# Performance work log

Measured on AMD Instinct MI355X. Metric: run time of the kernel, lower is better.

Reference implementation:

```python
import jax, jax.numpy as jnp
import numpy as np

E = 1024
H = 16
HD = E // H
FF = 4 * E
B, T = 2, 2048


def _linear_params(key, fan_in, fan_out):
    k1, k2 = jax.random.split(key)
    bound = 1.0 / np.sqrt(fan_in)
    W = jax.random.uniform(k1, (fan_out, fan_in), jnp.float32, -bound, bound)
    b = jax.random.uniform(k2, (fan_out,), jnp.float32, -bound, bound)
    return W, b


def setup_inputs() -> dict:
    key = jax.random.key(0)
    keys = jax.random.split(key, 8)
    x = jax.random.normal(keys[0], (B, T, E), jnp.float32)
    Wq, bq = _linear_params(keys[1], E, E)
    Wk, bk = _linear_params(keys[2], E, E)
    Wv, bv = _linear_params(keys[3], E, E)
    Wo, bo = _linear_params(keys[4], E, E)
    W1, b1 = _linear_params(keys[5], E, FF)
    W2, b2 = _linear_params(keys[6], FF, E)
    ln1_g = jnp.ones((E,), jnp.float32); ln1_b = jnp.zeros((E,), jnp.float32)
    ln2_g = jnp.ones((E,), jnp.float32); ln2_b = jnp.zeros((E,), jnp.float32)
    return {"x": x, "Wq": Wq, "bq": bq, "Wk": Wk, "bk": bk, "Wv": Wv, "bv": bv,
            "Wo": Wo, "bo": bo, "W1": W1, "b1": b1, "W2": W2, "b2": b2,
            "ln1_g": ln1_g, "ln1_b": ln1_b, "ln2_g": ln2_g, "ln2_b": ln2_b}


def _layernorm(x, g, b, eps=1e-5):
    mu = jnp.mean(x, axis=-1, keepdims=True)
    var = jnp.var(x, axis=-1, keepdims=True)
    return (x - mu) * jax.lax.rsqrt(var + eps) * g + b


def reference(x, Wq, bq, Wk, bk, Wv, bv, Wo, bo, W1, b1, W2, b2,
              ln1_g, ln1_b, ln2_g, ln2_b):
    Bc, Tc, Ec = x.shape
    h = _layernorm(x, ln1_g, ln1_b)
    # projections (torch Linear: y = x @ W.T + b)
    q = (h @ Wq.T + bq).reshape(Bc, Tc, H, HD).transpose(0, 2, 1, 3)  # [B,H,T,hd]
    k = (h @ Wk.T + bk).reshape(Bc, Tc, H, HD).transpose(0, 2, 1, 3)
    v = (h @ Wv.T + bv).reshape(Bc, Tc, H, HD).transpose(0, 2, 1, 3)
    scores = jnp.einsum('bhqd,bhkd->bhqk', q, k) / np.sqrt(HD).astype(np.float32)
    causal = jnp.tril(jnp.ones((Tc, Tc), bool))
    scores = jnp.where(causal, scores, -jnp.inf)
    att = jax.nn.softmax(scores, axis=-1)  # dropout = identity (eval)
    out = jnp.einsum('bhqk,bhkd->bhqd', att, v)
    out = out.transpose(0, 2, 1, 3).reshape(Bc, Tc, Ec)
    x = x + out @ Wo.T + bo
    h2 = _layernorm(x, ln2_g, ln2_b)
    ff = jax.nn.relu(h2 @ W1.T + b1) @ W2.T + b2
    return x + ff
```

## Files before the change

### kernel.cpp

```cpp
#include <hip/hip_runtime.h>

typedef unsigned short u16;
typedef __bf16 bf16x8 __attribute__((ext_vector_type(8)));
typedef float f32x4 __attribute__((ext_vector_type(4)));

#define E_ 1024
#define T_ 2048
#define B_ 2
#define H_ 16
#define FF_ 4096
#define M_ 4096

__device__ __forceinline__ u16 f2b(float f) {
    union { float f; unsigned u; } c; c.f = f;
    unsigned r = c.u + 0x7FFFu + ((c.u >> 16) & 1u);
    return (u16)(r >> 16);
}
__device__ __forceinline__ u16 f2bt(float f) {
    union { float f; unsigned u; } c; c.f = f;
    return (u16)(c.u >> 16);
}

__device__ __forceinline__ void gl16(const u16* g, u16* l) {
    __builtin_amdgcn_global_load_lds(
        (__attribute__((address_space(1))) void*)g,
        (__attribute__((address_space(3))) void*)l, 16, 0, 0);
}

template<int N> __device__ __forceinline__ void wait_vmcnt() {
    if constexpr (N == 2)      asm volatile("s_waitcnt vmcnt(2)" ::: "memory");
    else if constexpr (N == 3) asm volatile("s_waitcnt vmcnt(3)" ::: "memory");
    else if constexpr (N == 4) asm volatile("s_waitcnt vmcnt(4)" ::: "memory");
    else                       asm volatile("s_waitcnt vmcnt(0)" ::: "memory");
}

__global__ __launch_bounds__(256) void cvt_ln(
        const float* __restrict__ Wq, const float* __restrict__ Wk,
        const float* __restrict__ Wv, const float* __restrict__ Wo,
        const float* __restrict__ W1, const float* __restrict__ W2,
        const float* __restrict__ bq, const float* __restrict__ bk,
        const float* __restrict__ bv,
        u16* __restrict__ WqkvB, u16* __restrict__ WoB,
        u16* __restrict__ W1B, u16* __restrict__ W2B,
        float* __restrict__ bqkv,
        const float* __restrict__ x, const float* __restrict__ g1,
        const float* __restrict__ b1v, u16* __restrict__ hB) {
    if (blockIdx.x < 1024) {
        int row = blockIdx.x * 4 + (threadIdx.x >> 6);
        int t = threadIdx.x & 63;
        const float* xr = x + (size_t)row * E_;
        float v[16];
        float sum = 0.f, ss = 0.f;
#pragma unroll
        for (int c = 0; c < 4; c++) {
            float4 f = *(const float4*)&xr[c * 256 + t * 4];
            v[c * 4 + 0] = f.x; v[c * 4 + 1] = f.y; v[c * 4 + 2] = f.z; v[c * 4 + 3] = f.w;
            sum += f.x + f.y + f.z + f.w;
            ss += f.x * f.x + f.y * f.y + f.z * f.z + f.w * f.w;
        }
#pragma unroll
        for (int d = 32; d; d >>= 1) {
            sum += __shfl_xor(sum, d);
            ss  += __shfl_xor(ss, d);
        }
        float mu = sum * (1.f / E_);
        float var = ss * (1.f / E_) - mu * mu;
        float rs = rsqrtf(var + 1e-5f);
#pragma unroll
        for (int c = 0; c < 4; c++) {
            int idx = c * 256 + t * 4;
            float4 g4 = *(const float4*)&g1[idx];
            float4 b4 = *(const float4*)&b1v[idx];
            ushort4 o;
            o.x = f2b((v[c * 4 + 0] - mu) * rs * g4.x + b4.x);
            o.y = f2b((v[c * 4 + 1] - mu) * rs * g4.y + b4.y);
            o.z = f2b((v[c * 4 + 2] - mu) * rs * g4.z + b4.z);
            o.w = f2b((v[c * 4 + 3] - mu) * rs * g4.w + b4.w);
            *(ushort4*)&hB[(size_t)row * E_ + idx] = o;
        }
        return;
    }
    int i = (blockIdx.x - 1024) * 256 + threadIdx.x;
    if (i >= 3146496) return;
    if (i >= 3145728) {
        int j = i - 3145728;
        const float* s = (j < 256) ? bq : (j < 512) ? bk : bv;
        int jj = j & 255;
        *(float4*)&bqkv[j * 4] = *(const float4*)&s[jj * 4];
        return;
    }
    const float* src; u16* dst; int j;
    if (i < 786432) {
        src = (i < 262144) ? Wq : (i < 524288) ? Wk : Wv;
        j = i & 262143;
        dst = WqkvB + (i >> 18) * (E_ * E_);
    } else if (i < 1048576) { j = i - 786432;  src = Wo; dst = WoB; }
    else if (i < 2097152)   { j = i - 1048576; src = W1; dst = W1B; }
    else                    { j = i - 2097152; src = W2; dst = W2B; }
    float4 f = *(const float4*)&src[j * 4];
    ushort4 o;
    o.x = f2b(f.x); o.y = f2b(f.y); o.z = f2b(f.z); o.w = f2b(f.w);
    *(ushort4*)&dst[j * 4] = o;
}

__global__ __launch_bounds__(64) void ln_fwd(u16* __restrict__ out, const float* __restrict__ x,
                                             const float* __restrict__ g, const float* __restrict__ bta) {
    int row = blockIdx.x;
    int t = threadIdx.x;
    const float* xr = x + (size_t)row * E_;
    float v[16];
    float sum = 0.f, ss = 0.f;
#pragma unroll
    for (int c = 0; c < 4; c++) {
        float4 f = *(const float4*)&xr[c * 256 + t * 4];
        v[c * 4 + 0] = f.x; v[c * 4 + 1] = f.y; v[c * 4 + 2] = f.z; v[c * 4 + 3] = f.w;
        sum += f.x + f.y + f.z + f.w;
        ss += f.x * f.x + f.y * f.y + f.z * f.z + f.w * f.w;
    }
#pragma unroll
    for (int d = 32; d; d >>= 1) {
        sum += __shfl_xor(sum, d);
        ss  += __shfl_xor(ss, d);
    }
    float mu = sum * (1.f / E_);
    float var = ss * (1.f / E_) - mu * mu;
    float rs = rsqrtf(var + 1e-5f);
#pragma unroll
    for (int c = 0; c < 4; c++) {
        int idx = c * 256 + t * 4;
        float4 g4 = *(const float4*)&g[idx];
        float4 b4 = *(const float4*)&bta[idx];
        ushort4 o;
        o.x = f2b((v[c * 4 + 0] - mu) * rs * g4.x + b4.x);
        o.y = f2b((v[c * 4 + 1] - mu) * rs * g4.y + b4.y);
        o.z = f2b((v[c * 4 + 2] - mu) * rs * g4.z + b4.z);
        o.w = f2b((v[c * 4 + 3] - mu) * rs * g4.w + b4.w);
        *(ushort4*)&out[(size_t)row * E_ + idx] = o;
    }
}

template<int BM, int BN>
__global__ __launch_bounds__(256) void gemm_bt(
        const u16* __restrict__ A, const u16* __restrict__ Bt,
        const float* __restrict__ bias, const float* __restrict__ residual,
        float* __restrict__ outF, float* __restrict__ outF1,
        u16* __restrict__ outB, u16* __restrict__ outVt,
        int M, int N, int K, int ldk, int relu, int qkvmode) {
    constexpr int MT = BM / 32, NT = BN / 32;
    constexpr int LA = BM / 64, LB = BN / 64;
    __shared__ __align__(16) u16 As[3][BM * 32];
    __shared__ __align__(16) u16 Bs[3][BN * 32];
    int tid = threadIdx.x;
    int m0 = blockIdx.y * BM, n0 = blockIdx.x * BN;
    int kz = blockIdx.z;
    int koff = kz * K;
    int wave = tid >> 6, lane = tid & 63;
    int wm = wave & 1, wn = wave >> 1;
    int r16 = lane & 15, kg = lane >> 4;

    const u16* gA = A + (size_t)(m0 + wave * (BM / 4) + (lane >> 2)) * ldk + koff + (lane & 3) * 8;
    const u16* gB = Bt + (size_t)(n0 + wave * (BN / 4) + (lane >> 2)) * ldk + koff + (lane & 3) * 8;
    size_t row16 = (size_t)16 * ldk;
    int aoff = wave * (BM / 4) * 32;
    int boff = wave * (BN / 4) * 32;

    f32x4 acc[MT][NT] = {};

    const int nk = K >> 5;

    auto issue = [&](int kt, int buf) {
        int k1 = kt << 5;
        gl16(gA + k1, As[buf] + aoff);
        if (LA == 2) gl16(gA + k1 + row16, As[buf] + aoff + 512);
        gl16(gB + k1, Bs[buf] + boff);
        if (LB == 2) gl16(gB + k1 + row16, Bs[buf] + boff + 512);
    };

    auto compute = [&](int cb) {
        bf16x8 af[MT], bfr[NT];
#pragma unroll
        for (int mt = 0; mt < MT; mt++)
            af[mt] = *(const bf16x8*)&As[cb][(wm * (BM / 2) + mt * 16 + r16) * 32 + kg * 8];
#pragma unroll
        for (int nt = 0; nt < NT; nt++)
            bfr[nt] = *(const bf16x8*)&Bs[cb][(wn * (BN / 2) + nt * 16 + r16) * 32 + kg * 8];
#pragma unroll
        for (int mt = 0; mt < MT; mt++)
#pragma unroll
            for (int nt = 0; nt < NT; nt++)
                acc[mt][nt] = __builtin_amdgcn_mfma_f32_16x16x32_bf16(af[mt], bfr[nt], acc[mt][nt], 0, 0, 0);
    };

    issue(0, 0);
    issue(1, 1);

    int cur = 0;
    for (int ks = 0; ks < nk - 1; ks++) {
        wait_vmcnt<LA + LB>();
        __builtin_amdgcn_s_barrier();
        asm volatile("" ::: "memory");
        if (ks + 2 < nk) {
            int p2 = cur ? cur - 1 : 2;
            issue(ks + 2, p2);
        }
        compute(cur);
        cur = (cur < 2) ? cur + 1 : 0;
    }
    asm volatile("s_waitcnt vmcnt(0)" ::: "memory");
    __builtin_amdgcn_s_barrier();
    asm volatile("" ::: "memory");
    compute(cur);

#pragma unroll
    for (int mt = 0; mt < MT; mt++) {
#pragma unroll
        for (int nt = 0; nt < NT; nt++) {
            int gm = m0 + wm * (BM / 2) + mt * 16 + kg * 4;
            int gn = n0 + wn * (BN / 2) + nt * 16 + r16;
            float bv = bias[gn];
            if (qkvmode) {
                if (gn < 2048) {
                    float scl = (gn < 1024) ? 0.18033688f : 1.0f;
#pragma unroll
                    for (int r = 0; r < 4; r++)
                        outB[(size_t)(gm + r) * 2048 + gn] = f2b((acc[mt][nt][r] + bv) * scl);
                } else {
                    int bq_ = gm >> 11, tq = gm & 2047, d = gn - 2048;
                    ushort4 ov;
                    ov.x = f2b(acc[mt][nt][0] + bv);
                    ov.y = f2b(acc[mt][nt][1] + bv);
                    ov.z = f2b(acc[mt][nt][2] + bv);
                    ov.w = f2b(acc[mt][nt][3] + bv);
                    *(ushort4*)&outVt[((size_t)(bq_ * 1024 + d)) * 2048 + tq] = ov;
                }
            } else if (outF1) {
#pragma unroll
                for (int r = 0; r < 4; r++) {
                    size_t off = (size_t)(gm + r) * N + gn;
                    if (kz == 0) {
                        float v = acc[mt][nt][r] + bv;
                        if (residual) v += residual[off];
                        outF[off] = v;
                    } else {
                        outF1[off] = acc[mt][nt][r];
                    }
                }
            } else {
#pragma unroll
                for (int r = 0; r < 4; r++) {
                    float v = acc[mt][nt][r] + bv;
                    size_t off = (size_t)(gm + r) * N + gn;
                    if (residual) v += residual[off];
                    if (relu) v = fmaxf(v, 0.f);
                    if (outF) outF[off] = v;
                    else outB[off] = f2b(v);
                }
            }
        }
    }
}

__global__ __launch_bounds__(256) void addf4(float* __restrict__ d, const float* __restrict__ p) {
    size_t i = ((size_t)blockIdx.x * 256 + threadIdx.x) * 4;
    float4 a = *(float4*)&d[i];
    float4 b = *(const float4*)&p[i];
    a.x += b.x; a.y += b.y; a.z += b.z; a.w += b.w;
    *(float4*)&d[i] = a;
}

#define AST 68
__global__ __launch_bounds__(256) void attn_mfma(
        const u16* __restrict__ qk, const u16* __restrict__ vt,
        u16* __restrict__ out) {
    __shared__ __align__(16) u16 Ks[2][64 * AST];
    __shared__ __align__(16) u16 Vs[2][64 * AST];
    __shared__ __align__(16) u16 Ps[4][16 * AST];

    int bz = blockIdx.x;
    int h  = bz & 15;
    int b  = (bz >> 4) & 1;
    int qt = bz >> 5;

    int tid = threadIdx.x;
    int w = tid >> 6, lane = tid & 63;
    int g = lane >> 4, l16 = lane & 15;

    int qrow = qt * 64 + w * 16 + l16;
    bf16x8 qf[2];
    qf[0] = *(const bf16x8*)&qk[(size_t)(b * T_ + qrow) * 2048 + h * 64 + g * 8];
    qf[1] = *(const bf16x8*)&qk[(size_t)(b * T_ + qrow) * 2048 + h * 64 + 32 + g * 8];

    f32x4 o[4] = {};
    f32x4 lp = {0.f, 0.f, 0.f, 0.f};

    int r1 = tid >> 3, col1 = (tid & 7) * 8;
    const u16* gK = qk + (size_t)(b * T_) * 2048 + 1024 + h * 64;
    const u16* gV = vt + (size_t)(b * 1024 + h * 64) * 2048;

    uint4 kr1 = *(const uint4*)&gK[(size_t)r1 * 2048 + col1];
    uint4 kr2 = *(const uint4*)&gK[(size_t)(r1 + 32) * 2048 + col1];
    uint4 vr1 = *(const uint4*)&gV[(size_t)r1 * 2048 + col1];
    uint4 vr2 = *(const uint4*)&gV[(size_t)(r1 + 32) * 2048 + col1];

    for (int t = 0; t <= qt; t++) {
        int cur = t & 1;
        *(uint4*)&Ks[cur][r1 * AST + col1] = kr1;
        *(uint4*)&Ks[cur][(r1 + 32) * AST + col1] = kr2;
        *(uint4*)&Vs[cur][r1 * AST + col1] = vr1;
        *(uint4*)&Vs[cur][(r1 + 32) * AST + col1] = vr2;
        __syncthreads();
        if (t < qt) {
            int j1 = (t + 1) * 64;
            kr1 = *(const uint4*)&gK[(size_t)(j1 + r1) * 2048 + col1];
            kr2 = *(const uint4*)&gK[(size_t)(j1 + r1 + 32) * 2048 + col1];
            vr1 = *(const uint4*)&gV[(size_t)r1 * 2048 + j1 + col1];
            vr2 = *(const uint4*)&gV[(size_t)(r1 + 32) * 2048 + j1 + col1];
        }

        f32x4 s[4];
#pragma unroll
        for (int nt = 0; nt < 4; nt++) {
            f32x4 c16 = {-16.f, -16.f, -16.f, -16.f};
            bf16x8 k0 = *(const bf16x8*)&Ks[cur][(nt * 16 + l16) * AST + g * 8];
            bf16x8 k1 = *(const bf16x8*)&Ks[cur][(nt * 16 + l16) * AST + 32 + g * 8];
            s[nt] = __builtin_amdgcn_mfma_f32_16x16x32_bf16(qf[0], k0, c16, 0, 0, 0);
            s[nt] = __builtin_amdgcn_mfma_f32_16x16x32_bf16(qf[1], k1, s[nt], 0, 0, 0);
        }

        if (t == qt) {
            int j0 = t * 64;
#pragma unroll
            for (int nt = 0; nt < 4; nt++) {
                int key = j0 + nt * 16 + l16;
#pragma unroll
                for (int r = 0; r < 4; r++) {
                    int q = qt * 64 + w * 16 + g * 4 + r;
                    if (key > q) s[nt][r] = -INFINITY;
                }
            }
        }

#pragma unroll
        for (int nt = 0; nt < 4; nt++)
#pragma unroll
            for (int r = 0; r < 4; r++) {
                float p = exp2f(s[nt][r]);
                lp[r] += p;
                Ps[w][(g * 4 + r) * AST + nt * 16 + l16] = f2bt(p);
            }

#pragma unroll
        for (int kf = 0; kf < 2; kf++) {
            bf16x8 pf = *(const bf16x8*)&Ps[w][l16 * AST + kf * 32 + g * 8];
#pragma unroll
            for (int nt = 0; nt < 4; nt++) {
                bf16x8 vf = *(const bf16x8*)&Vs[cur][(nt * 16 + l16) * AST + kf * 32 + g * 8];
                o[nt] = __builtin_amdgcn_mfma_f32_16x16x32_bf16(pf, vf, o[nt], 0, 0, 0);
            }
        }
    }

#pragma unroll
    for (int x = 1; x <= 8; x <<= 1)
#pragma unroll
        for (int r = 0; r < 4; r++)
            lp[r] += __shfl_xor(lp[r], x);

    float inv[4];
#pragma unroll
    for (int r = 0; r < 4; r++) inv[r] = 1.f / lp[r];
    int qg = qt * 64 + w * 16 + g * 4;
#pragma unroll
    for (int nt = 0; nt < 4; nt++)
#pragma unroll
        for (int r = 0; r < 4; r++)
            out[(size_t)(b * T_ + qg + r) * E_ + h * 64 + nt * 16 + l16] =
                f2b(o[nt][r] * inv[r]);
}

extern "C" void kernel_launch(void* const* d_in, const int* in_sizes, int n_in,
                              void* d_out, int out_size, void* d_ws, size_t ws_size,
                              hipStream_t stream) {
    const float* x    = (const float*)d_in[0];
    const float* Wq   = (const float*)d_in[1];
    const float* bq   = (const float*)d_in[2];
    const float* Wk   = (const float*)d_in[3];
    const float* bk   = (const float*)d_in[4];
    const float* Wv   = (const float*)d_in[5];
    const float* bv   = (const float*)d_in[6];
    const float* Wo   = (const float*)d_in[7];
    const float* bo   = (const float*)d_in[8];
    const float* W1   = (const float*)d_in[9];
    const float* b1   = (const float*)d_in[10];
    const float* W2   = (const float*)d_in[11];
    const float* b2   = (const float*)d_in[12];
    const float* ln1g = (const float*)d_in[13];
    const float* ln1b = (const float*)d_in[14];
    const float* ln2g = (const float*)d_in[15];
    const float* ln2b = (const float*)d_in[16];

    char* ws = (char*)d_ws;
    size_t off = 0;
    auto alloc = [&](size_t bytes) { char* p = ws + off; off += (bytes + 255) & ~(size_t)255; return p; };

    u16*   hB    = (u16*)  alloc((size_t)M_ * E_ * 2);
    u16*   WqkvB = (u16*)  alloc((size_t)3 * E_ * E_ * 2);
    u16*   WoB   = (u16*)  alloc((size_t)E_ * E_ * 2);
    u16*   W1B   = (u16*)  alloc((size_t)FF_ * E_ * 2);
    u16*   W2B   = (u16*)  alloc((size_t)E_ * FF_ * 2);
    float* bqkv  = (float*)alloc(3 * E_ * 4);
    u16*   qkB   = (u16*)  alloc((size_t)M_ * 2 * E_ * 2);
    u16*   vtG   = (u16*)  alloc((size_t)M_ * E_ * 2);
    u16*   attnB = (u16*)  alloc((size_t)M_ * E_ * 2);
    float* x2    = (float*)alloc((size_t)M_ * E_ * 4);
    u16*   h2B   = (u16*)  alloc((size_t)M_ * E_ * 2);
    u16*   rB    = (u16*)  alloc((size_t)M_ * FF_ * 2);
    float* P1    = (float*)alloc((size_t)M_ * E_ * 4);

    cvt_ln<<<1024 + 12291, 256, 0, stream>>>(Wq, Wk, Wv, Wo, W1, W2, bq, bk, bv,
                                             WqkvB, WoB, W1B, W2B, bqkv,
                                             x, ln1g, ln1b, hB);

    gemm_bt<128, 128><<<dim3(3 * E_ / 128, M_ / 128), 256, 0, stream>>>(
        hB, WqkvB, bqkv, nullptr, nullptr, nullptr, qkB, vtG, M_, 3 * E_, E_, E_, 0, 1);

    attn_mfma<<<B_ * H_ * (T_ / 64), 256, 0, stream>>>(qkB, vtG, attnB);

    gemm_bt<64, 128><<<dim3(E_ / 128, M_ / 64), 256, 0, stream>>>(
        attnB, WoB, bo, x, x2, nullptr, nullptr, nullptr, M_, E_, E_, E_, 0, 0);

    ln_fwd<<<M_, 64, 0, stream>>>(h2B, x2, ln2g, ln2b);

    gemm_bt<128, 128><<<dim3(FF_ / 128, M_ / 128), 256, 0, stream>>>(
        h2B, W1B, b1, nullptr, nullptr, nullptr, rB, nullptr, M_, FF_, E_, E_, 1, 0);

    gemm_bt<64, 128><<<dim3(E_ / 128, M_ / 64, 2), 256, 0, stream>>>(
        rB, W2B, b2, x2, (float*)d_out, P1, nullptr, nullptr, M_, E_, FF_ / 2, FF_, 0, 0);

    addf4<<<(M_ * E_) / (256 * 4), 256, 0, stream>>>((float*)d_out, P1);
}
```

Measured before the change: 387.3 us.

## Split FFN down-projection 4-way over K with 128x128 tiles and swizzle blocks

The second FFN GEMM moves from a 2-way K split with 64x128 tiles to a 4-way K split with 128x128 tiles. Partial sums go to three scratch buffers that reuse dead workspace (the qk buffer and the start of the workspace), and a three-input add kernel replaces the two-input add. An XCD-style block-index swizzle is also enabled for the FFN up-projection and down-projection GEMMs to improve L2 locality. The extra partial buffers add memory traffic in the reduction pass. Aliasing P3 onto the workspace start (hB, the first weight buffers) depends on those buffers no longer being needed at that point.

```diff
diff --git a/kernel.cpp b/kernel.cpp
--- a/kernel.cpp
+++ b/kernel.cpp
@@ -143,15 +143,24 @@
 __global__ __launch_bounds__(256) void gemm_bt(
         const u16* __restrict__ A, const u16* __restrict__ Bt,
         const float* __restrict__ bias, const float* __restrict__ residual,
-        float* __restrict__ outF, float* __restrict__ outF1,
+        float* __restrict__ outF, float* __restrict__ oP1,
+        float* __restrict__ oP2, float* __restrict__ oP3,
         u16* __restrict__ outB, u16* __restrict__ outVt,
-        int M, int N, int K, int ldk, int relu, int qkvmode) {
+        int M, int N, int K, int ldk, int relu, int qkvmode, int swz) {
     constexpr int MT = BM / 32, NT = BN / 32;
     constexpr int LA = BM / 64, LB = BN / 64;
     __shared__ __align__(16) u16 As[3][BM * 32];
     __shared__ __align__(16) u16 Bs[3][BN * 32];
     int tid = threadIdx.x;
-    int m0 = blockIdx.y * BM, n0 = blockIdx.x * BN;
+    int bx = blockIdx.x, by = blockIdx.y;
+    if (swz) {
+        int gx = gridDim.x;
+        int nwg = gx * gridDim.y;
+        int lin = by * gx + bx;
+        int w = (lin & 7) * (nwg >> 3) + (lin >> 3);
+        bx = w % gx; by = w / gx;
+    }
+    int m0 = by * BM, n0 = bx * BN;
     int kz = blockIdx.z;
     int koff = kz * K;
     int wave = tid >> 6, lane = tid & 63;
@@ -233,7 +242,8 @@
                     ov.w = f2b(acc[mt][nt][3] + bv);
                     *(ushort4*)&outVt[((size_t)(bq_ * 1024 + d)) * 2048 + tq] = ov;
                 }
-            } else if (outF1) {
+            } else if (oP1) {
+                float* po = (kz == 1) ? oP1 : (kz == 2) ? oP2 : oP3;
 #pragma unroll
                 for (int r = 0; r < 4; r++) {
                     size_t off = (size_t)(gm + r) * N + gn;
@@ -242,7 +252,7 @@
                         if (residual) v += residual[off];
                         outF[off] = v;
                     } else {
-                        outF1[off] = acc[mt][nt][r];
+                        po[off] = acc[mt][nt][r];
                     }
                 }
             } else {
@@ -260,12 +270,18 @@
     }
 }
 
-__global__ __launch_bounds__(256) void addf4(float* __restrict__ d, const float* __restrict__ p) {
+__global__ __launch_bounds__(256) void addf3(float* __restrict__ d, const float* __restrict__ a,
+                                             const float* __restrict__ b, const float* __restrict__ c) {
     size_t i = ((size_t)blockIdx.x * 256 + threadIdx.x) * 4;
-    float4 a = *(float4*)&d[i];
-    float4 b = *(const float4*)&p[i];
-    a.x += b.x; a.y += b.y; a.z += b.z; a.w += b.w;
-    *(float4*)&d[i] = a;
+    float4 vd = *(float4*)&d[i];
+    float4 va = *(const float4*)&a[i];
+    float4 vb = *(const float4*)&b[i];
+    float4 vc = *(const float4*)&c[i];
+    vd.x += va.x + vb.x + vc.x;
+    vd.y += va.y + vb.y + vc.y;
+    vd.z += va.z + vb.z + vc.z;
+    vd.w += va.w + vb.w + vc.w;
+    *(float4*)&d[i] = vd;
 }
 
 #define AST 68
@@ -416,26 +432,32 @@
     u16*   h2B   = (u16*)  alloc((size_t)M_ * E_ * 2);
     u16*   rB    = (u16*)  alloc((size_t)M_ * FF_ * 2);
     float* P1    = (float*)alloc((size_t)M_ * E_ * 4);
+    float* P2 = (float*)qkB;
+    float* P3 = (float*)ws;
 
     cvt_ln<<<1024 + 12291, 256, 0, stream>>>(Wq, Wk, Wv, Wo, W1, W2, bq, bk, bv,
                                              WqkvB, WoB, W1B, W2B, bqkv,
                                              x, ln1g, ln1b, hB);
 
     gemm_bt<128, 128><<<dim3(3 * E_ / 128, M_ / 128), 256, 0, stream>>>(
-        hB, WqkvB, bqkv, nullptr, nullptr, nullptr, qkB, vtG, M_, 3 * E_, E_, E_, 0, 1);
+        hB, WqkvB, bqkv, nullptr, nullptr, nullptr, nullptr, nullptr, qkB, vtG,
+        M_, 3 * E_, E_, E_, 0, 1, 0);
 
     attn_mfma<<<B_ * H_ * (T_ / 64), 256, 0, stream>>>(qkB, vtG, attnB);
 
     gemm_bt<64, 128><<<dim3(E_ / 128, M_ / 64), 256, 0, stream>>>(
-        attnB, WoB, bo, x, x2, nullptr, nullptr, nullptr, M_, E_, E_, E_, 0, 0);
+        attnB, WoB, bo, x, x2, nullptr, nullptr, nullptr, nullptr, nullptr,
+        M_, E_, E_, E_, 0, 0, 0);
 
     ln_fwd<<<M_, 64, 0, stream>>>(h2B, x2, ln2g, ln2b);
 
     gemm_bt<128, 128><<<dim3(FF_ / 128, M_ / 128), 256, 0, stream>>>(
-        h2B, W1B, b1, nullptr, nullptr, nullptr, rB, nullptr, M_, FF_, E_, E_, 1, 0);
-
-    gemm_bt<64, 128><<<dim3(E_ / 128, M_ / 64, 2), 256, 0, stream>>>(
-        rB, W2B, b2, x2, (float*)d_out, P1, nullptr, nullptr, M_, E_, FF_ / 2, FF_, 0, 0);
-
-    addf4<<<(M_ * E_) / (256 * 4), 256, 0, stream>>>((float*)d_out, P1);
-}
+        h2B, W1B, b1, nullptr, nullptr, nullptr, nullptr, nullptr, rB, nullptr,
+        M_, FF_, E_, E_, 1, 0, 1);
+
+    gemm_bt<128, 128><<<dim3(E_ / 128, M_ / 128, 4), 256, 0, stream>>>(
+        rB, W2B, b2, x2, (float*)d_out, P1, P2, P3, nullptr, nullptr,
+        M_, E_, FF_ / 4, FF_, 0, 0, 1);
+
+    addf3<<<(M_ * E_) / (256 * 4), 256, 0, stream>>>((float*)d_out, P1, P2, P3);
+}
```

Result: no change. 387.3 us (median of 2 runs) (-0.0%).
